# Kernel optimization log

Hardware: AMD Instinct MI355X
Metric: run time of the kernel (lower is better)

## Reference

```python
import jax, jax.numpy as jnp
import numpy as np

N_LAYERS, D_MODEL, H, D_K, D_V, D_FF, VOCAB = 6, 512, 8, 64, 64, 2048, 32000
B, S = 4, 512
NEG_INF = -jnp.inf


def positional_encoding(seq_len, d_model):
    # Faithful to the (buggy-vs-paper) source: angle = pos / 10000**(2*i/d_model),
    # sin for even i, cos for odd i (i is the raw channel index).
    pos = jnp.arange(seq_len, dtype=jnp.float32)[:, None]
    i = jnp.arange(d_model, dtype=jnp.float32)[None, :]
    angle = pos / jnp.power(10000.0, 2.0 * i / d_model)
    return jnp.where((jnp.arange(d_model) % 2 == 0)[None, :], jnp.sin(angle), jnp.cos(angle))


def layer_norm(x, g, b, eps=1e-5):
    mu = jnp.mean(x, -1, keepdims=True)
    var = jnp.mean((x - mu) ** 2, -1, keepdims=True)
    return (x - mu) * jax.lax.rsqrt(var + eps) * g + b


def mha(q_in, k_in, v_in, wq, wk, wv, wo, q_mask, k_mask, causal):
    # wq/wk: (H, D, D_K), wv: (H, D, D_V), wo: (H*D_V, D)
    q = jnp.einsum('bsd,hdk->bhsk', q_in, wq)
    k = jnp.einsum('btd,hdk->bhtk', k_in, wk)
    v = jnp.einsum('btd,hdk->bhtk', v_in, wv)
    scores = jnp.einsum('bhsk,bhtk->bhst', q, k) / jnp.sqrt(jnp.float32(D_K))
    allowed = q_mask[:, None, :, None] & k_mask[:, None, None, :]  # (B,1,S,T)
    if causal:
        sl, tl = q_in.shape[1], k_in.shape[1]
        allowed = allowed & (jnp.arange(tl)[None, :] <= jnp.arange(sl)[:, None])[None, None]
    scores = jnp.where(allowed, scores, NEG_INF)
    attn = jax.nn.softmax(scores, axis=-1)
    out = jnp.einsum('bhst,bhtk->bshk', attn, v)  # (B,S,H,D_V)
    out = out.reshape(out.shape[0], out.shape[1], H * D_V)
    return out @ wo


def ffn(x, w1, b1, w2, b2):
    return jax.nn.relu(x @ w1 + b1) @ w2 + b2


def setup_inputs() -> dict:
    key = jax.random.key(0)
    ks = iter(jax.random.split(key, 40))
    f = lambda shape, scale: (jax.random.normal(next(ks), shape, dtype=jnp.float32) * scale)
    inp = {
        'src_tokens': jax.random.randint(next(ks), (B, S), 0, VOCAB),
        'tgt_tokens': jax.random.randint(next(ks), (B, S), 0, VOCAB),
        'src_mask': jnp.ones((B, S), dtype=bool),
        'tgt_mask': jnp.ones((B, S), dtype=bool),
        'embed': f((VOCAB, D_MODEL), 0.02),
        'enc_wqkv': f((N_LAYERS, 3, H, D_MODEL, D_K), 0.04),
        'enc_wo': f((N_LAYERS, H * D_V, D_MODEL), 0.04),
        'enc_ff_w1': f((N_LAYERS, D_MODEL, D_FF), 0.02),
        'enc_ff_b1': jnp.zeros((N_LAYERS, D_FF), jnp.float32),
        'enc_ff_w2': f((N_LAYERS, D_FF, D_MODEL), 0.02),
        'enc_ff_b2': jnp.zeros((N_LAYERS, D_MODEL), jnp.float32),
        'enc_ln_g': jnp.ones((N_LAYERS, 2, D_MODEL), jnp.float32),
        'enc_ln_b': jnp.zeros((N_LAYERS, 2, D_MODEL), jnp.float32),
        'dec_wqkv1': f((N_LAYERS, 3, H, D_MODEL, D_K), 0.04),
        'dec_wo1': f((N_LAYERS, H * D_V, D_MODEL), 0.04),
        'dec_wqkv2': f((N_LAYERS, 3, H, D_MODEL, D_K), 0.04),
        'dec_wo2': f((N_LAYERS, H * D_V, D_MODEL), 0.04),
        'dec_ff_w1': f((N_LAYERS, D_MODEL, D_FF), 0.02),
        'dec_ff_b1': jnp.zeros((N_LAYERS, D_FF), jnp.float32),
        'dec_ff_w2': f((N_LAYERS, D_FF, D_MODEL), 0.02),
        'dec_ff_b2': jnp.zeros((N_LAYERS, D_MODEL), jnp.float32),
        'dec_ln_g': jnp.ones((N_LAYERS, 3, D_MODEL), jnp.float32),
        'dec_ln_b': jnp.zeros((N_LAYERS, 3, D_MODEL), jnp.float32),
        'out_w': f((D_MODEL, VOCAB), 0.02),
        'out_b': jnp.zeros((VOCAB,), jnp.float32),
    }
    return inp


def reference(src_tokens, tgt_tokens, src_mask, tgt_mask, embed,
              enc_wqkv, enc_wo, enc_ff_w1, enc_ff_b1, enc_ff_w2, enc_ff_b2, enc_ln_g, enc_ln_b,
              dec_wqkv1, dec_wo1, dec_wqkv2, dec_wo2, dec_ff_w1, dec_ff_b1, dec_ff_w2, dec_ff_b2,
              dec_ln_g, dec_ln_b, out_w, out_b):
    pe = positional_encoding(src_tokens.shape[1], D_MODEL)
    x = embed[src_tokens] + pe[None]
    for i in range(N_LAYERS):
        a = mha(x, x, x, enc_wqkv[i, 0], enc_wqkv[i, 1], enc_wqkv[i, 2], enc_wo[i], src_mask, src_mask, False)
        x = layer_norm(x + a, enc_ln_g[i, 0], enc_ln_b[i, 0])
        x = layer_norm(x + ffn(x, enc_ff_w1[i], enc_ff_b1[i], enc_ff_w2[i], enc_ff_b2[i]), enc_ln_g[i, 1], enc_ln_b[i, 1])
    pe_t = positional_encoding(tgt_tokens.shape[1], D_MODEL)
    y = embed[tgt_tokens] + pe_t[None]
    for i in range(N_LAYERS):
        a = mha(y, y, y, dec_wqkv1[i, 0], dec_wqkv1[i, 1], dec_wqkv1[i, 2], dec_wo1[i], tgt_mask, tgt_mask, True)
        y = layer_norm(y + a, dec_ln_g[i, 0], dec_ln_b[i, 0])
        a = mha(y, x, x, dec_wqkv2[i, 0], dec_wqkv2[i, 1], dec_wqkv2[i, 2], dec_wo2[i], tgt_mask, src_mask, False)
        y = layer_norm(y + a, dec_ln_g[i, 1], dec_ln_b[i, 1])
        y = layer_norm(y + ffn(y, dec_ff_w1[i], dec_ff_b1[i], dec_ff_w2[i], dec_ff_b2[i]), dec_ln_g[i, 2], dec_ln_b[i, 2])
    return y @ out_w + out_b
```

## Files before the change

kernel.cpp:

```cpp
#include <hip/hip_runtime.h>
#include <math.h>


typedef unsigned short u16;
typedef __attribute__((ext_vector_type(8))) short short8;
typedef __attribute__((ext_vector_type(4))) float f32x4;

__device__ __forceinline__ u16 f2bf(float f){
  unsigned u = __float_as_uint(f);
  return (u16)((u + 0x7fffu + ((u >> 16) & 1u)) >> 16);
}

#define GLDS16(gp, lp) __builtin_amdgcn_global_load_lds( \
    (const __attribute__((address_space(1))) unsigned int*)(const void*)(gp), \
    (__attribute__((address_space(3))) unsigned int*)(void*)(lp), 16, 0, 0)

__global__ __launch_bounds__(256) void embed_pe_kernel(
    const int* __restrict__ tok, const float* __restrict__ emb,
    float* __restrict__ out, u16* __restrict__ outh)
{
  int row = blockIdx.x;
  int s = row & 511;
  int t = tok[row];
  #pragma unroll
  for (int j = 0; j < 2; j++){
    int d = threadIdx.x + 256*j;
    float ang = (float)s * powf(10000.0f, -2.0f*(float)d/512.0f);
    float pe = (d & 1) ? cosf(ang) : sinf(ang);
    float v = emb[(size_t)t*512 + d] + pe;
    out[(size_t)row*512 + d] = v;
    outh[(size_t)row*512 + d] = f2bf(v);
  }
}

struct WDesc { const float* W; unsigned long long gs, ds; u16* dst; int K; int nx; int end; };
struct WPack { WDesc d[6]; };

__global__ __launch_bounds__(256) void wcast_multi(WPack P, int nseg){
  int blk = blockIdx.x, s = 0;
  while (s < nseg-1 && blk >= P.d[s].end) s++;
  WDesc D = P.d[s];
  int base = s ? P.d[s-1].end : 0;
  int lb = blk - base;
  int g = lb % D.nx, kt = lb / D.nx;
  __shared__ u16 T[64][65];
  int tid = threadIdx.x;
  const float* Wb = D.W + (size_t)g*D.gs + (size_t)kt*64*D.ds;
  #pragma unroll
  for (int i = 0; i < 16; i++){
    int li = tid + 256*i;
    int kk = li >> 6, c = li & 63;
    T[kk][c] = f2bf(Wb[(size_t)kk*D.ds + c]);
  }
  __syncthreads();
  #pragma unroll
  for (int i = 0; i < 16; i++){
    int lo = tid + 256*i;
    int c = lo >> 6, kk = lo & 63;
    D.dst[(size_t)(g*64 + c)*D.K + kt*64 + kk] = T[kk][c];
  }
}

__global__ __launch_bounds__(256) void vtrans_kernel(
    const u16* __restrict__ qkv, u16* __restrict__ vT)
{
  int z = blockIdx.x >> 3, tt = blockIdx.x & 7;
  int b = z >> 3, h = z & 7;
  __shared__ u16 T[64][65];
  int tid = threadIdx.x;
  const u16* src = qkv + (size_t)(b*512 + tt*64)*1536 + 1024 + h*64;
  #pragma unroll
  for (int i = 0; i < 16; i++){
    int li = tid + 256*i; int r = li >> 6, c = li & 63;
    T[r][c] = src[(size_t)r*1536 + c];
  }
  __syncthreads();
  #pragma unroll
  for (int i = 0; i < 16; i++){
    int lo = tid + 256*i; int d = lo >> 6, r = lo & 63;
    vT[(size_t)(z*64 + d)*512 + tt*64 + r] = T[r][d];
  }
}

__global__ __launch_bounds__(256) void flash_attn_kernel(
    const u16* __restrict__ qkv, const u16* __restrict__ vT,
    u16* __restrict__ ctx, int causal)
{
  __shared__ __align__(16) u16 lQ[64*64];
  __shared__ __align__(16) u16 lK[2][64*64];
  __shared__ __align__(16) u16 lV[2][64*64];
  __shared__ __align__(16) u16 lP[4][16*64];
  int tid = threadIdx.x, lane = tid & 63, w = tid >> 6;
  int r16 = lane & 15, l4 = lane >> 4;
  int bh = blockIdx.x >> 3, qb = blockIdx.x & 7;
  int b = bh >> 3, h = bh & 7;
  const u16* qbase = qkv + (size_t)b*512*1536 + h*64;

  #pragma unroll
  for (int i = 0; i < 2; i++){
    int idx = i*256 + tid;
    int r = idx >> 3, c = idx & 7;
    GLDS16(qbase + (size_t)(qb*64 + r)*1536 + ((c ^ (r & 7))*8),
           lQ + (i*256 + w*64)*8);
  }
  auto stageKV = [&](int buf, int tt){
    #pragma unroll
    for (int i = 0; i < 2; i++){
      int idx = i*256 + tid;
      int r = idx >> 3, c = idx & 7;
      GLDS16(qbase + 512 + (size_t)(tt*64 + r)*1536 + ((c ^ (r & 7))*8),
             lK[buf] + (i*256 + w*64)*8);
      GLDS16(vT + ((size_t)bh*64 + r)*512 + tt*64 + ((c ^ (r & 7))*8),
             lV[buf] + (i*256 + w*64)*8);
    }
  };
  stageKV(0, 0);
  __syncthreads();
  short8 qa[2];
  #pragma unroll
  for (int kt = 0; kt < 2; kt++){
    int q = w*16 + r16;
    qa[kt] = *(const short8*)&lQ[q*64 + (((kt*4 + l4) ^ (q & 7))*8)];
  }

  f32x4 o[4];
  float mrow[4], lrow[4];
  #pragma unroll
  for (int j = 0; j < 4; j++){ o[j] = (f32x4){0.f,0.f,0.f,0.f}; mrow[j] = -3e38f; lrow[j] = 0.f; }

  int ntl = causal ? (qb + 1) : 8;
  int buf = 0;
  for (int tt = 0; tt < ntl; tt++){
    if (tt + 1 < ntl) stageKV(buf ^ 1, tt + 1);
    f32x4 s[4];
    #pragma unroll
    for (int ct = 0; ct < 4; ct++) s[ct] = (f32x4){0.f,0.f,0.f,0.f};
    #pragma unroll
    for (int kt = 0; kt < 2; kt++){
      #pragma unroll
      for (int ct = 0; ct < 4; ct++){
        int trow = ct*16 + r16;
        short8 kb = *(const short8*)&lK[buf][trow*64 + (((kt*4 + l4) ^ (trow & 7))*8)];
        s[ct] = __builtin_amdgcn_mfma_f32_16x16x32_bf16(qa[kt], kb, s[ct], 0, 0, 0);
      }
    }
    float p[4][4];
    #pragma unroll
    for (int ct = 0; ct < 4; ct++)
      #pragma unroll
      for (int r = 0; r < 4; r++){
        float v = s[ct][r] * 0.125f;
        if (causal && tt == qb && (ct*16 + r16) > (w*16 + l4*4 + r)) v = -1e30f;
        p[ct][r] = v;
      }
    #pragma unroll
    for (int r = 0; r < 4; r++){
      float pm = fmaxf(fmaxf(p[0][r], p[1][r]), fmaxf(p[2][r], p[3][r]));
      #pragma unroll
      for (int off = 1; off < 16; off <<= 1) pm = fmaxf(pm, __shfl_xor(pm, off));
      float mn = fmaxf(mrow[r], pm);
      float scl = __expf(mrow[r] - mn);
      mrow[r] = mn;
      float rs = 0.f;
      #pragma unroll
      for (int ct = 0; ct < 4; ct++){ p[ct][r] = __expf(p[ct][r] - mn); rs += p[ct][r]; }
      #pragma unroll
      for (int off = 1; off < 16; off <<= 1) rs += __shfl_xor(rs, off);
      lrow[r] = lrow[r]*scl + rs;
      #pragma unroll
      for (int jf = 0; jf < 4; jf++) o[jf][r] *= scl;
    }
    u16* myP = &lP[w][0];
    #pragma unroll
    for (int ct = 0; ct < 4; ct++)
      #pragma unroll
      for (int r = 0; r < 4; r++){
        int q = l4*4 + r, t = ct*16 + r16;
        myP[q*64 + (((t >> 3) ^ (q & 7))*8) + (t & 7)] = f2bf(p[ct][r]);
      }
    #pragma unroll
    for (int kt = 0; kt < 2; kt++){
      short8 pa = *(const short8*)&myP[r16*64 + (((kt*4 + l4) ^ (r16 & 7))*8)];
      #pragma unroll
      for (int jf = 0; jf < 4; jf++){
        int dr = jf*16 + r16;
        short8 vv = *(const short8*)&lV[buf][dr*64 + (((kt*4 + l4) ^ (dr & 7))*8)];
        o[jf] = __builtin_amdgcn_mfma_f32_16x16x32_bf16(pa, vv, o[jf], 0, 0, 0);
      }
    }
    __syncthreads();
    buf ^= 1;
  }
  #pragma unroll
  for (int r = 0; r < 4; r++){
    float inv = 1.0f / lrow[r];
    int q = qb*64 + w*16 + l4*4 + r;
    u16* dst = ctx + (size_t)(b*512 + q)*512 + h*64;
    #pragma unroll
    for (int jf = 0; jf < 4; jf++)
      dst[jf*16 + r16] = f2bf(o[jf][r] * inv);
  }
}

__global__ __launch_bounds__(256) void ln_kernel(
    float* __restrict__ x, const float* __restrict__ res,
    const float* __restrict__ g, const float* __restrict__ bt,
    u16* __restrict__ xh)
{
  int tid = threadIdx.x, lane = tid & 63, wv = tid >> 6;
  int row = blockIdx.x*4 + wv;
  size_t base = (size_t)row*512;
  float v[8]; float sum = 0.f;
  #pragma unroll
  for (int j = 0; j < 8; j++){
    int d = lane + 64*j;
    v[j] = x[base + d] + res[base + d];
    sum += v[j];
  }
  #pragma unroll
  for (int o = 32; o; o >>= 1) sum += __shfl_xor(sum, o);
  float mu = sum * (1.0f/512.0f);
  float vs = 0.f;
  #pragma unroll
  for (int j = 0; j < 8; j++){ float dd = v[j] - mu; vs += dd*dd; }
  #pragma unroll
  for (int o = 32; o; o >>= 1) vs += __shfl_xor(vs, o);
  float rstd = rsqrtf(vs*(1.0f/512.0f) + 1e-5f);
  #pragma unroll
  for (int j = 0; j < 8; j++){
    int d = lane + 64*j;
    float ov = (v[j] - mu)*rstd*g[d] + bt[d];
    x[base + d] = ov;
    xh[base + d] = f2bf(ov);
  }
}

template<int BM, int BN, int WM, int WN>
__global__ __launch_bounds__(WM*WN*64) void mfma_gemm(
    const u16* __restrict__ A, int lda,
    const u16* __restrict__ B, int ldb,
    void* __restrict__ C, int ldc, int cbf,
    const float* __restrict__ bias, int relu, int K)
{
  constexpr int NT  = WM*WN*64;
  constexpr int SM  = BM/WM, SN = BN/WN;
  constexpr int FM  = SM/16, FN = SN/16;
  constexpr int RPS = NT/8;
  constexpr int AG  = BM/RPS, BG = BN/RPS;
  __shared__ __align__(16) u16 lA[2][BM*64];
  __shared__ __align__(16) u16 lB[2][BN*64];
  int tid = threadIdx.x, lane = tid & 63, w = tid >> 6;
  int wm = w / WN, wn = w % WN;
  int r16 = lane & 15, l4 = lane >> 4;
  int sr = (w << 3) + (lane >> 3);
  int sc = lane & 7;
  int scs = sc ^ (sr & 7);
  const u16* Ab = A + (size_t)blockIdx.y*BM*lda + (size_t)sr*lda + scs*8;
  const u16* Bb = B + (size_t)blockIdx.x*BN*ldb + (size_t)sr*ldb + scs*8;
  f32x4 acc[FM][FN];
  #pragma unroll
  for (int i = 0; i < FM; i++)
    #pragma unroll
    for (int j = 0; j < FN; j++)
      acc[i][j] = (f32x4){0.f, 0.f, 0.f, 0.f};

  auto stage = [&](int buf, int kt){
    #pragma unroll
    for (int s = 0; s < AG; s++)
      GLDS16(Ab + (size_t)(s*RPS)*lda + kt, &lA[buf][(s*RPS + (w << 3))*64]);
    #pragma unroll
    for (int s = 0; s < BG; s++)
      GLDS16(Bb + (size_t)(s*RPS)*ldb + kt, &lB[buf][(s*RPS + (w << 3))*64]);
  };
  stage(0, 0);
  int nk = K >> 6, cur = 0;
  for (int kt = 0; kt < nk; kt++){
    __syncthreads();
    if (kt + 1 < nk) stage(cur ^ 1, (kt + 1) << 6);
    #pragma unroll
    for (int ks = 0; ks < 2; ks++){
      short8 av[FM], bv[FN];
      #pragma unroll
      for (int i = 0; i < FM; i++){
        int row = wm*SM + i*16 + r16;
        av[i] = *(const short8*)&lA[cur][row*64 + (((ks*4 + l4) ^ (row & 7))*8)];
      }
      #pragma unroll
      for (int j = 0; j < FN; j++){
        int row = wn*SN + j*16 + r16;
        bv[j] = *(const short8*)&lB[cur][row*64 + (((ks*4 + l4) ^ (row & 7))*8)];
      }
      #pragma unroll
      for (int i = 0; i < FM; i++)
        #pragma unroll
        for (int j = 0; j < FN; j++)
          acc[i][j] = __builtin_amdgcn_mfma_f32_16x16x32_bf16(av[i], bv[j], acc[i][j], 0, 0, 0);
    }
    cur ^= 1;
  }

  int m0 = blockIdx.y*BM + wm*SM, n0 = blockIdx.x*BN + wn*SN;
  int r4 = l4*4;
  #pragma unroll
  for (int i = 0; i < FM; i++){
    #pragma unroll
    for (int j = 0; j < FN; j++){
      int col = n0 + j*16 + r16;
      float bi = bias ? bias[col] : 0.f;
      #pragma unroll
      for (int r = 0; r < 4; r++){
        int rowg = m0 + i*16 + r4 + r;
        float o = acc[i][j][r] + bi;
        if (relu) o = fmaxf(o, 0.f);
        if (cbf) ((u16*)C)[(size_t)rowg*ldc + col] = f2bf(o);
        else     ((float*)C)[(size_t)rowg*ldc + col] = o;
      }
    }
  }
}

extern "C" void kernel_launch(void* const* d_in, const int* in_sizes, int n_in,
                              void* d_out, int out_size, void* d_ws, size_t ws_size,
                              hipStream_t stream)
{
  (void)in_sizes; (void)n_in; (void)out_size; (void)ws_size;
  const int*   src_tok   = (const int*)  d_in[0];
  const int*   tgt_tok   = (const int*)  d_in[1];
  const float* emb       = (const float*)d_in[4];
  const float* enc_wqkv  = (const float*)d_in[5];
  const float* enc_wo    = (const float*)d_in[6];
  const float* enc_ff_w1 = (const float*)d_in[7];
  const float* enc_ff_b1 = (const float*)d_in[8];
  const float* enc_ff_w2 = (const float*)d_in[9];
  const float* enc_ff_b2 = (const float*)d_in[10];
  const float* enc_ln_g  = (const float*)d_in[11];
  const float* enc_ln_b  = (const float*)d_in[12];
  const float* dec_wqkv1 = (const float*)d_in[13];
  const float* dec_wo1   = (const float*)d_in[14];
  const float* dec_wqkv2 = (const float*)d_in[15];
  const float* dec_wo2   = (const float*)d_in[16];
  const float* dec_ff_w1 = (const float*)d_in[17];
  const float* dec_ff_b1 = (const float*)d_in[18];
  const float* dec_ff_w2 = (const float*)d_in[19];
  const float* dec_ff_b2 = (const float*)d_in[20];
  const float* dec_ln_g  = (const float*)d_in[21];
  const float* dec_ln_b  = (const float*)d_in[22];
  const float* out_w     = (const float*)d_in[23];
  const float* out_b     = (const float*)d_in[24];
  float* outp = (float*)d_out;

  const size_t MB = 1024*1024;
  char* wsb = (char*)d_ws;
  float* xb     = (float*)(wsb + 0*MB);
  float* yb     = (float*)(wsb + 4*MB);
  u16*   xh     = (u16*)  (wsb + 8*MB);
  u16*   ctxb   = (u16*)  (wsb + 10*MB);
  u16*   yh     = (u16*)  (wsb + 12*MB);
  u16*   qkvb   = (u16*)  (wsb + 14*MB);
  u16*   vT     = (u16*)  (wsb + 20*MB);
  u16*   hid    = (u16*)  (wsb + 14*MB);
  u16*   sQKV   = (u16*)  (wsb + 22*MB);
  u16*   sWO    = (u16*)  (wsb + 23*MB + 512*1024);
  u16*   sFF1   = (u16*)  (wsb + 24*MB);
  u16*   sFF2   = (u16*)  (wsb + 26*MB);
  float* proj   = (float*)(wsb + 28*MB);
  u16*   wvbuf  = (u16*)  (wsb + 0*MB);

  auto g64 = [&](const u16* A,int lda,const u16* B,int ldb,void* C,int ldc,
                 int cbf,const float* bias,int relu,int M,int N,int K){
    mfma_gemm<64,64,2,2><<<dim3(N/64, M/64), 256, 0, stream>>>(
        A,lda,B,ldb,C,ldc,cbf,bias,relu,K);
  };
  auto g128 = [&](const u16* A,int lda,const u16* B,int ldb,void* C,int ldc,
                  int cbf,const float* bias,int relu,int M,int N,int K){
    mfma_gemm<128,128,2,4><<<dim3(N/128, M/128), 512, 0, stream>>>(
        A,lda,B,ldb,C,ldc,cbf,bias,relu,K);
  };
  auto ln = [&](float* x, const float* g, const float* b, u16* oh){
    ln_kernel<<<512, 256, 0, stream>>>(x, proj, g, b, oh);
  };
  auto attn = [&](int causal){
    vtrans_kernel<<<256, 256, 0, stream>>>(qkvb, vT);
    flash_attn_kernel<<<256, 256, 0, stream>>>(qkvb, vT, ctxb, causal);
  };
  auto cast = [&](WDesc* segs, int n){
    WPack P; int tot = 0;
    for (int s = 0; s < n; s++){
      tot += segs[s].nx * (segs[s].K/64);
      segs[s].end = tot;
      P.d[s] = segs[s];
    }
    for (int s = n; s < 6; s++) P.d[s] = P.d[0];
    wcast_multi<<<tot, 256, 0, stream>>>(P, n);
  };

  const size_t WQKV_L = (size_t)3*8*512*64;

  embed_pe_kernel<<<2048, 256, 0, stream>>>(src_tok, emb, xb, xh);
  for (int i = 0; i < 6; i++){
    WDesc segs[4] = {
      {enc_wqkv + i*WQKV_L,            32768, 64,   sQKV, 512,  24, 0},
      {enc_wo   + (size_t)i*262144,    64,    512,  sWO,  512,  8,  0},
      {enc_ff_w1+ (size_t)i*512*2048,  64,    2048, sFF1, 512,  32, 0},
      {enc_ff_w2+ (size_t)i*2048*512,  64,    512,  sFF2, 2048, 8,  0}};
    cast(segs, 4);
    g64(xh, 512, sQKV, 512, qkvb, 1536, 1, nullptr, 0, 2048, 1536, 512);
    attn(0);
    g64(ctxb, 512, sWO, 512, proj, 512, 0, nullptr, 0, 2048, 512, 512);
    ln(xb, enc_ln_g + i*1024,       enc_ln_b + i*1024,       xh);
    g64(xh, 512, sFF1, 512, hid, 2048, 1, enc_ff_b1 + i*2048, 1, 2048, 2048, 512);
    g64(hid, 2048, sFF2, 2048, proj, 512, 0, enc_ff_b2 + i*512, 0, 2048, 512, 2048);
    ln(xb, enc_ln_g + i*1024 + 512, enc_ln_b + i*1024 + 512, xh);
  }

  embed_pe_kernel<<<2048, 256, 0, stream>>>(tgt_tok, emb, yb, yh);
  for (int i = 0; i < 6; i++){
    WDesc segs1[4] = {
      {dec_wqkv1 + i*WQKV_L,           32768, 64,   sQKV, 512,  24, 0},
      {dec_wo1   + (size_t)i*262144,   64,    512,  sWO,  512,  8,  0},
      {dec_ff_w1 + (size_t)i*512*2048, 64,    2048, sFF1, 512,  32, 0},
      {dec_ff_w2 + (size_t)i*2048*512, 64,    512,  sFF2, 2048, 8,  0}};
    cast(segs1, 4);
    g64(yh, 512, sQKV, 512, qkvb, 1536, 1, nullptr, 0, 2048, 1536, 512);
    attn(1);
    g64(ctxb, 512, sWO, 512, proj, 512, 0, nullptr, 0, 2048, 512, 512);
    ln(yb, dec_ln_g + i*1536,        dec_ln_b + i*1536,        yh);
    WDesc segs2[2] = {
      {dec_wqkv2 + i*WQKV_L,         32768, 64,  sQKV, 512, 24, 0},
      {dec_wo2   + (size_t)i*262144, 64,    512, sWO,  512, 8,  0}};
    cast(segs2, 2);
    g64(yh, 512, sQKV, 512, qkvb, 1536, 1, nullptr, 0, 2048, 512, 512);
    g64(xh, 512, sQKV + (size_t)512*512, 512, qkvb + 512, 1536, 1, nullptr, 0,
        2048, 1024, 512);
    attn(0);
    g64(ctxb, 512, sWO, 512, proj, 512, 0, nullptr, 0, 2048, 512, 512);
    ln(yb, dec_ln_g + i*1536 + 512,  dec_ln_b + i*1536 + 512,  yh);
    g64(yh, 512, sFF1, 512, hid, 2048, 1, dec_ff_b1 + i*2048, 1, 2048, 2048, 512);
    g64(hid, 2048, sFF2, 2048, proj, 512, 0, dec_ff_b2 + i*512, 0, 2048, 512, 2048);
    ln(yb, dec_ln_g + i*1536 + 1024, dec_ln_b + i*1536 + 1024, yh);
  }

  const int c0s[5] = {0, 8192, 16384, 24576, 32000};
  for (int c = 0; c < 4; c++){
    int c0 = c0s[c], NC = c0s[c+1] - c0;
    WDesc seg[1] = {{out_w + c0, 64, 32000, wvbuf, 512, NC/64, 0}};
    cast(seg, 1);
    g128(yh, 512, wvbuf, 512, outp + c0, 32000, 0, out_b + c0, 0, 2048, NC, 512);
  }
}
```

Measured before the change: 1.535 ms.

## Retune GEMM tiles, add MFMA priority hints, fuse cross-attention QKV GEMMs

Wraps the MFMA blocks in the attention and GEMM kernels with s_setprio raises so matrix issue gets wave priority. It changes the GEMM warp layouts to fewer waves per block (64x64 with 2 waves, 128x128 with 4 waves). It switches the QKV and FF1 projections to 128x128 tiles. It replaces the two cross-attention projection GEMMs with a single launch that picks the A source per z-slice. Together these aim to cut launch count and improve per-wave MFMA utilisation, at the cost of fewer resident waves and more tail imbalance on the larger tiles.

```diff
diff --git a/kernel.cpp b/kernel.cpp
--- a/kernel.cpp
+++ b/kernel.cpp
@@ -135,6 +135,7 @@
     f32x4 s[4];
     #pragma unroll
     for (int ct = 0; ct < 4; ct++) s[ct] = (f32x4){0.f,0.f,0.f,0.f};
+    __builtin_amdgcn_s_setprio(1);
     #pragma unroll
     for (int kt = 0; kt < 2; kt++){
       #pragma unroll
@@ -144,6 +145,7 @@
         s[ct] = __builtin_amdgcn_mfma_f32_16x16x32_bf16(qa[kt], kb, s[ct], 0, 0, 0);
       }
     }
+    __builtin_amdgcn_s_setprio(0);
     float p[4][4];
     #pragma unroll
     for (int ct = 0; ct < 4; ct++)
@@ -178,6 +180,7 @@
         int q = l4*4 + r, t = ct*16 + r16;
         myP[q*64 + (((t >> 3) ^ (q & 7))*8) + (t & 7)] = f2bf(p[ct][r]);
       }
+    __builtin_amdgcn_s_setprio(1);
     #pragma unroll
     for (int kt = 0; kt < 2; kt++){
       short8 pa = *(const short8*)&myP[r16*64 + (((kt*4 + l4) ^ (r16 & 7))*8)];
@@ -188,6 +191,7 @@
         o[jf] = __builtin_amdgcn_mfma_f32_16x16x32_bf16(pa, vv, o[jf], 0, 0, 0);
       }
     }
+    __builtin_amdgcn_s_setprio(0);
     __syncthreads();
     buf ^= 1;
   }
@@ -290,11 +294,13 @@
         int row = wn*SN + j*16 + r16;
         bv[j] = *(const short8*)&lB[cur][row*64 + (((ks*4 + l4) ^ (row & 7))*8)];
       }
+      __builtin_amdgcn_s_setprio(1);
       #pragma unroll
       for (int i = 0; i < FM; i++)
         #pragma unroll
         for (int j = 0; j < FN; j++)
           acc[i][j] = __builtin_amdgcn_mfma_f32_16x16x32_bf16(av[i], bv[j], acc[i][j], 0, 0, 0);
+      __builtin_amdgcn_s_setprio(0);
     }
     cur ^= 1;
   }
@@ -317,6 +323,80 @@
       }
     }
   }
+}
+
+__global__ __launch_bounds__(128) void xattn_qkv_gemm(
+    const u16* __restrict__ Ay, const u16* __restrict__ Ax,
+    const u16* __restrict__ Bt, u16* __restrict__ C)
+{
+  constexpr int BM=64, BN=64, WM=2, WN=1, NT=128;
+  constexpr int SM=BM/WM, SN=BN/WN, FM=SM/16, FN=SN/16, RPS=NT/8;
+  constexpr int AG=BM/RPS, BG=BN/RPS;
+  __shared__ __align__(16) u16 lA[2][BM*64];
+  __shared__ __align__(16) u16 lB[2][BN*64];
+  int tid = threadIdx.x, lane = tid & 63, w = tid >> 6;
+  int wm = w, wn = 0;
+  int r16 = lane & 15, l4 = lane >> 4;
+  int sr = (w << 3) + (lane >> 3);
+  int sc = lane & 7;
+  int scs = sc ^ (sr & 7);
+  int z = blockIdx.z;
+  const u16* A = (z == 0) ? Ay : Ax;
+  const u16* Ab = A + (size_t)blockIdx.y*BM*512 + (size_t)sr*512 + scs*8;
+  const u16* Bb = Bt + (size_t)(z*512 + blockIdx.x*BN)*512 + (size_t)sr*512 + scs*8;
+  f32x4 acc[FM][FN];
+  #pragma unroll
+  for (int i = 0; i < FM; i++)
+    #pragma unroll
+    for (int j = 0; j < FN; j++)
+      acc[i][j] = (f32x4){0.f, 0.f, 0.f, 0.f};
+  auto stage = [&](int buf, int kt){
+    #pragma unroll
+    for (int s = 0; s < AG; s++)
+      GLDS16(Ab + (size_t)(s*RPS)*512 + kt, &lA[buf][(s*RPS + (w << 3))*64]);
+    #pragma unroll
+    for (int s = 0; s < BG; s++)
+      GLDS16(Bb + (size_t)(s*RPS)*512 + kt, &lB[buf][(s*RPS + (w << 3))*64]);
+  };
+  stage(0, 0);
+  int cur = 0;
+  for (int kt = 0; kt < 8; kt++){
+    __syncthreads();
+    if (kt + 1 < 8) stage(cur ^ 1, (kt + 1) << 6);
+    #pragma unroll
+    for (int ks = 0; ks < 2; ks++){
+      short8 av[FM], bv[FN];
+      #pragma unroll
+      for (int i = 0; i < FM; i++){
+        int row = wm*SM + i*16 + r16;
+        av[i] = *(const short8*)&lA[cur][row*64 + (((ks*4 + l4) ^ (row & 7))*8)];
+      }
+      #pragma unroll
+      for (int j = 0; j < FN; j++){
+        int row = wn*SN + j*16 + r16;
+        bv[j] = *(const short8*)&lB[cur][row*64 + (((ks*4 + l4) ^ (row & 7))*8)];
+      }
+      __builtin_amdgcn_s_setprio(1);
+      #pragma unroll
+      for (int i = 0; i < FM; i++)
+        #pragma unroll
+        for (int j = 0; j < FN; j++)
+          acc[i][j] = __builtin_amdgcn_mfma_f32_16x16x32_bf16(av[i], bv[j], acc[i][j], 0, 0, 0);
+      __builtin_amdgcn_s_setprio(0);
+    }
+    cur ^= 1;
+  }
+  int m0 = blockIdx.y*BM + wm*SM, n0 = z*512 + blockIdx.x*BN + wn*SN;
+  int r4 = l4*4;
+  #pragma unroll
+  for (int i = 0; i < FM; i++)
+    #pragma unroll
+    for (int j = 0; j < FN; j++)
+      #pragma unroll
+      for (int r = 0; r < 4; r++){
+        int rowg = m0 + i*16 + r4 + r;
+        C[(size_t)rowg*1536 + n0 + j*16 + r16] = f2bf(acc[i][j][r]);
+      }
 }
 
 extern "C" void kernel_launch(void* const* d_in, const int* in_sizes, int n_in,
@@ -368,12 +448,12 @@
 
   auto g64 = [&](const u16* A,int lda,const u16* B,int ldb,void* C,int ldc,
                  int cbf,const float* bias,int relu,int M,int N,int K){
-    mfma_gemm<64,64,2,2><<<dim3(N/64, M/64), 256, 0, stream>>>(
+    mfma_gemm<64,64,2,1><<<dim3(N/64, M/64), 128, 0, stream>>>(
         A,lda,B,ldb,C,ldc,cbf,bias,relu,K);
   };
   auto g128 = [&](const u16* A,int lda,const u16* B,int ldb,void* C,int ldc,
                   int cbf,const float* bias,int relu,int M,int N,int K){
-    mfma_gemm<128,128,2,4><<<dim3(N/128, M/128), 512, 0, stream>>>(
+    mfma_gemm<128,128,2,2><<<dim3(N/128, M/128), 256, 0, stream>>>(
         A,lda,B,ldb,C,ldc,cbf,bias,relu,K);
   };
   auto ln = [&](float* x, const float* g, const float* b, u16* oh){
@@ -404,11 +484,11 @@
       {enc_ff_w1+ (size_t)i*512*2048,  64,    2048, sFF1, 512,  32, 0},
       {enc_ff_w2+ (size_t)i*2048*512,  64,    512,  sFF2, 2048, 8,  0}};
     cast(segs, 4);
-    g64(xh, 512, sQKV, 512, qkvb, 1536, 1, nullptr, 0, 2048, 1536, 512);
+    g128(xh, 512, sQKV, 512, qkvb, 1536, 1, nullptr, 0, 2048, 1536, 512);
     attn(0);
     g64(ctxb, 512, sWO, 512, proj, 512, 0, nullptr, 0, 2048, 512, 512);
     ln(xb, enc_ln_g + i*1024,       enc_ln_b + i*1024,       xh);
-    g64(xh, 512, sFF1, 512, hid, 2048, 1, enc_ff_b1 + i*2048, 1, 2048, 2048, 512);
+    g128(xh, 512, sFF1, 512, hid, 2048, 1, enc_ff_b1 + i*2048, 1, 2048, 2048, 512);
     g64(hid, 2048, sFF2, 2048, proj, 512, 0, enc_ff_b2 + i*512, 0, 2048, 512, 2048);
     ln(xb, enc_ln_g + i*1024 + 512, enc_ln_b + i*1024 + 512, xh);
   }
@@ -421,7 +501,7 @@
       {dec_ff_w1 + (size_t)i*512*2048, 64,    2048, sFF1, 512,  32, 0},
       {dec_ff_w2 + (size_t)i*2048*512, 64,    512,  sFF2, 2048, 8,  0}};
     cast(segs1, 4);
-    g64(yh, 512, sQKV, 512, qkvb, 1536, 1, nullptr, 0, 2048, 1536, 512);
+    g128(yh, 512, sQKV, 512, qkvb, 1536, 1, nullptr, 0, 2048, 1536, 512);
     attn(1);
     g64(ctxb, 512, sWO, 512, proj, 512, 0, nullptr, 0, 2048, 512, 512);
     ln(yb, dec_ln_g + i*1536,        dec_ln_b + i*1536,        yh);
@@ -429,13 +509,11 @@
       {dec_wqkv2 + i*WQKV_L,         32768, 64,  sQKV, 512, 24, 0},
       {dec_wo2   + (size_t)i*262144, 64,    512, sWO,  512, 8,  0}};
     cast(segs2, 2);
-    g64(yh, 512, sQKV, 512, qkvb, 1536, 1, nullptr, 0, 2048, 512, 512);
-    g64(xh, 512, sQKV + (size_t)512*512, 512, qkvb + 512, 1536, 1, nullptr, 0,
-        2048, 1024, 512);
+    xattn_qkv_gemm<<<dim3(8, 32, 3), 128, 0, stream>>>(yh, xh, sQKV, qkvb);
     attn(0);
     g64(ctxb, 512, sWO, 512, proj, 512, 0, nullptr, 0, 2048, 512, 512);
     ln(yb, dec_ln_g + i*1536 + 512,  dec_ln_b + i*1536 + 512,  yh);
-    g64(yh, 512, sFF1, 512, hid, 2048, 1, dec_ff_b1 + i*2048, 1, 2048, 2048, 512);
+    g128(yh, 512, sFF1, 512, hid, 2048, 1, dec_ff_b1 + i*2048, 1, 2048, 2048, 512);
     g64(hid, 2048, sFF2, 2048, proj, 512, 0, dec_ff_b2 + i*512, 0, 2048, 512, 2048);
     ln(yb, dec_ln_g + i*1536 + 1024, dec_ln_b + i*1536 + 1024, yh);
   }
```

Result: slower. 1.730 ms (+12.7%).
